# Kernel tuning notes

Measured on AMD Instinct MI355X. Metric: run time of the kernel, lower is better.

## Reference

```python
import jax, jax.numpy as jnp
import numpy as np

EPS = 1e-5

def _relu6(x):
    return jnp.clip(x, 0.0, 6.0)

def _bn(x, g, b, m, v):
    # inference-mode batchnorm folded into scale/shift
    inv = g / jnp.sqrt(v + EPS)
    return x * inv[None, :, None, None] + (b - m * inv)[None, :, None, None]

def _patch_pw(x, W):
    # per-patch 1x1 conv. x: [B,Ci,H,Wd], W: [B,Fh,Fw,Co,Ci]
    B, C, H, Wd = x.shape
    Fh, Fw = W.shape[1:3]
    ph, pw = H // Fh, Wd // Fw
    xb = x.reshape(B, C, Fh, ph, Fw, pw)
    yb = jnp.einsum('bfgoc,bcfpgq->bofpgq', W, xb)
    return yb.reshape(B, W.shape[3], H, Wd)

def _patch_dw3(x, K):
    # per-patch depthwise 3x3, reflect pad applied to the full map (halo from neighbors).
    # x: [B,C,H,Wd], K: [B,Fh,Fw,C,3,3]
    B, C, H, Wd = x.shape
    Fh, Fw = K.shape[1:3]
    ph, pw = H // Fh, Wd // Fw
    xp = jnp.pad(x, ((0, 0), (0, 0), (1, 1), (1, 1)), mode='reflect')
    acc = jnp.zeros((B, C, Fh, ph, Fw, pw), x.dtype)
    for dy in range(3):
        for dx in range(3):
            xs = xp[:, :, dy:dy + H, dx:dx + Wd].reshape(B, C, Fh, ph, Fw, pw)
            k = K[:, :, :, :, dy, dx].transpose(0, 3, 1, 2)  # [B,C,Fh,Fw]
            acc = acc + xs * k[:, :, :, None, :, None]
    return acc.reshape(B, C, H, Wd)

def setup_inputs() -> dict:
    key = jax.random.key(0)
    ks = jax.random.split(key, 16)
    B, Cin, H, Wd = 4, 64, 128, 128
    hidden, Cout, Fh, Fw = 384, 64, 16, 16
    n_params = hidden * Cin + hidden * 9 + Cout * hidden  # 52608
    return {
        'x': jax.random.normal(ks[0], (B, Cin, H, Wd), jnp.float32),
        'w': jax.random.normal(ks[1], (B, n_params, Fh, Fw), jnp.float32) * 0.05,
        'g1': jax.random.uniform(ks[2], (hidden,), jnp.float32),
        'b1': jax.random.normal(ks[3], (hidden,), jnp.float32),
        'm1': jax.random.normal(ks[4], (hidden,), jnp.float32),
        'v1': jax.random.uniform(ks[5], (hidden,), jnp.float32),
        'g2': jax.random.uniform(ks[6], (hidden,), jnp.float32),
        'b2': jax.random.normal(ks[7], (hidden,), jnp.float32),
        'm2': jax.random.normal(ks[8], (hidden,), jnp.float32),
        'v2': jax.random.uniform(ks[9], (hidden,), jnp.float32),
        'g3': jax.random.uniform(ks[10], (Cout,), jnp.float32),
        'b3': jax.random.normal(ks[11], (Cout,), jnp.float32),
        'm3': jax.random.normal(ks[12], (Cout,), jnp.float32),
        'v3': jax.random.uniform(ks[13], (Cout,), jnp.float32),
    }

def reference(x, w, g1, b1, m1, v1, g2, b2, m2, v2, g3, b3, m3, v3):
    B, Cin = x.shape[:2]
    Fh, Fw = w.shape[2:]
    hidden = g1.shape[0]
    Cout = g3.shape[0]
    n1 = hidden * Cin
    n2 = hidden * 9
    wg = w.transpose(0, 2, 3, 1)  # [B,Fh,Fw,P]
    W1 = wg[..., :n1].reshape(B, Fh, Fw, hidden, Cin)
    K2 = wg[..., n1:n1 + n2].reshape(B, Fh, Fw, hidden, 3, 3)
    W3 = wg[..., n1 + n2:].reshape(B, Fh, Fw, Cout, hidden)
    h = _relu6(_bn(_patch_pw(x, W1), g1, b1, m1, v1))
    h = _relu6(_bn(_patch_dw3(h, K2), g2, b2, m2, v2))
    h = _bn(_patch_pw(h, W3), g3, b3, m3, v3)
    return x + h  # use_res_connect: stride==1 and in_nc==out_nc
```

## Files before the change

kernel.cpp:

```cpp
#include <hip/hip_runtime.h>

#define EPSV 1e-5f

constexpr int CIN = 64, NH = 128, NW = 128, HID = 384, COUT = 64;
constexpr int N1 = HID * CIN;
constexpr int N2 = HID * 9;
constexpr int NP = N1 + N2 + COUT * HID;

using bf16x8 = __attribute__((ext_vector_type(8))) short;
using f32x4  = __attribute__((ext_vector_type(4))) float;

__device__ __forceinline__ unsigned short f2bf(float f) {
  unsigned int u = __float_as_uint(f);
  u = (u + 0x7fffu + ((u >> 16) & 1u)) >> 16;
  return (unsigned short)u;
}
__device__ __forceinline__ unsigned int pack2(float a, float b) {
  return (unsigned int)f2bf(a) | ((unsigned int)f2bf(b) << 16);
}
__device__ __forceinline__ float ulo(unsigned int u) { return __uint_as_float(u << 16); }
__device__ __forceinline__ float uhi(unsigned int u) { return __uint_as_float(u & 0xffff0000u); }
__device__ __forceinline__ float clamp6(float v) { return fminf(fmaxf(v, 0.f), 6.f); }

#define BAR_LDS()                                             \
  do {                                                        \
    asm volatile("s_waitcnt lgkmcnt(0)" ::: "memory");        \
    __builtin_amdgcn_s_barrier();                             \
  } while (0)

__global__ __launch_bounds__(256) void k0_transpose(
    const float* __restrict__ x, unsigned short* __restrict__ xT) {
  __shared__ unsigned short xls[64][66];
  const int t = threadIdx.x;
  const int xh = blockIdx.x, y = blockIdx.y, b = blockIdx.z;
#pragma unroll
  for (int it = 0; it < 4; ++it) {
    int i = it * 256 + t;
    int xq = i & 15, c = i >> 4;
    float4 v = *reinterpret_cast<const float4*>(
        &x[((size_t)(b * CIN + c) * NH + y) * NW + xh * 64 + xq * 4]);
    *(unsigned int*)&xls[c][xq * 4]     = pack2(v.x, v.y);
    *(unsigned int*)&xls[c][xq * 4 + 2] = pack2(v.z, v.w);
  }
  __syncthreads();
#pragma unroll
  for (int it = 0; it < 4; ++it) {
    int i = it * 256 + t;
    int cq = i & 15, px = i >> 4;
    ushort4 o;
    o.x = xls[cq * 4 + 0][px];
    o.y = xls[cq * 4 + 1][px];
    o.z = xls[cq * 4 + 2][px];
    o.w = xls[cq * 4 + 3][px];
    *reinterpret_cast<ushort4*>(
        &xT[((size_t)(b * NH + y) * NW + xh * 64 + px) * 64 + cq * 4]) = o;
  }
}

__global__ __launch_bounds__(256) void k1_pw1(
    const float* __restrict__ w, const unsigned short* __restrict__ xT,
    const float* __restrict__ g1, const float* __restrict__ b1,
    const float* __restrict__ m1, const float* __restrict__ v1,
    unsigned short* __restrict__ h1T) {
  __shared__ unsigned short Wpk[2048 * 8];

  const unsigned int id = blockIdx.x;
  const int fbq = id & 7;
  const unsigned int rest = id >> 3;
  const int hgrp = rest % 24, q = rest / 24;
  const int fb = q * 8 + fbq;
  const int f = fb & 15, b = fb >> 4;
  const int h0 = hgrp * 16;

  const int t = threadIdx.x;
  const int lane = t & 63, wv = t >> 6;
  const int quad = lane >> 4, nn = lane & 15;
  const int pxi = wv * 16 + nn;

#pragma unroll
  for (int it = 0; it < 8; ++it) {
    int i = it * 256 + t;
    int gq = i & 3, cp = (i >> 2) & 31, hid = i >> 7;
    const float* wp =
        &w[((size_t)b * NP + (h0 + hid) * CIN + cp * 2) * 256 + f * 16 + gq * 4];
    float4 A  = *reinterpret_cast<const float4*>(wp);
    float4 Bv = *reinterpret_cast<const float4*>(wp + 256);
    int kc = cp >> 4, qd = (cp >> 2) & 3, j = (cp & 3) * 2;
    int hs = hid ^ (2 * qd) ^ gq;
    const float* Af = (const float*)&A;
    const float* Bf = (const float*)&Bv;
#pragma unroll
    for (int k = 0; k < 4; ++k) {
      int g = gq * 4 + k;
      *(unsigned int*)&Wpk[(((g * 2 + kc) * 4 + qd) * 16 + hs) * 8 + j] =
          pack2(Af[k], Bf[k]);
    }
  }

  float iv1[4], sh1[4];
#pragma unroll
  for (int jj = 0; jj < 4; ++jj) {
    int hid = h0 + quad * 4 + jj;
    float iv = g1[hid] * rsqrtf(v1[hid] + EPSV);
    iv1[jj] = iv;
    sh1[jj] = b1[hid] - m1[hid] * iv;
  }
  __syncthreads();

  const int y = f * 8 + (pxi >> 3);
  const size_t rowbase = ((size_t)b * NH + y) * NW;

  for (int g = 0; g < 16; ++g) {
    const int xc = g * 8 + (pxi & 7);
    const unsigned short* xp = &xT[(rowbase + xc) * 64];
    f32x4 acc = {0.f, 0.f, 0.f, 0.f};
    const int hs = nn ^ (2 * quad) ^ (g >> 2);
#pragma unroll
    for (int kc = 0; kc < 2; ++kc) {
      bf16x8 af = *reinterpret_cast<const bf16x8*>(
          &Wpk[(((g * 2 + kc) * 4 + quad) * 16 + hs) * 8]);
      bf16x8 bfr = *reinterpret_cast<const bf16x8*>(&xp[kc * 32 + quad * 8]);
      acc = __builtin_amdgcn_mfma_f32_16x16x32_bf16(af, bfr, acc, 0, 0, 0);
    }
    ushort4 o;
    o.x = f2bf(clamp6(acc[0] * iv1[0] + sh1[0]));
    o.y = f2bf(clamp6(acc[1] * iv1[1] + sh1[1]));
    o.z = f2bf(clamp6(acc[2] * iv1[2] + sh1[2]));
    o.w = f2bf(clamp6(acc[3] * iv1[3] + sh1[3]));
    *reinterpret_cast<ushort4*>(&h1T[(rowbase + xc) * HID + h0 + quad * 4]) = o;
  }
}

__global__ __launch_bounds__(256, 2) void k2_fused(
    const float* __restrict__ x, const float* __restrict__ w,
    const float* __restrict__ g2, const float* __restrict__ b2v,
    const float* __restrict__ m2, const float* __restrict__ v2,
    const float* __restrict__ g3, const float* __restrict__ b3v,
    const float* __restrict__ m3, const float* __restrict__ v3,
    const unsigned short* __restrict__ h1T, float* __restrict__ out) {
  __shared__ unsigned short tile[10][34][40];
  __shared__ unsigned short h2s[256][40];
  __shared__ unsigned short W3p[512 * 8];
  __shared__ unsigned short k2w[4][9][40];
  __shared__ float iv2s[HID], sh2s[HID];

  const unsigned int id = blockIdx.x;
  const int fbq = id & 7;
  const unsigned int rest = id >> 3;
  const int gang = rest & 7, q = rest >> 3;
  const int fb = q * 8 + fbq;
  const int f = fb & 15, b = fb >> 4;
  const int gq = gang >> 1, ch = gang & 1;
  const int c0 = gq * 32;

  const int t = threadIdx.x;
  const int lane = t & 63, wv = t >> 6;
  const int quad = lane >> 4, nn = lane & 15;

  for (int i = t; i < HID; i += 256) {
    float iv = g2[i] * rsqrtf(v2[i] + EPSV);
    iv2s[i] = iv;
    sh2s[i] = b2v[i] - m2[i] * iv;
  }

  float iv3[2][4], sh3[2][4];
#pragma unroll
  for (int cot = 0; cot < 2; ++cot)
#pragma unroll
    for (int jj = 0; jj < 4; ++jj) {
      int co = ch * 32 + cot * 16 + quad * 4 + jj;
      float iv = g3[co] * rsqrtf(v3[co] + EPSV);
      iv3[cot][jj] = iv;
      sh3[cot][jj] = b3v[co] - m3[co] * iv;
    }

  f32x4 acc[2][4];
#pragma unroll
  for (int cot = 0; cot < 2; ++cot)
#pragma unroll
    for (int nt = 0; nt < 4; ++nt) acc[cot][nt] = (f32x4){0.f, 0.f, 0.f, 0.f};

  const int glt = t >> 6, rt = (t >> 3) & 7, ct = t & 7;

#define TGEOM(IDX, SRC, DST)                                          \
  {                                                                   \
    int qh = (IDX) & 3, pxid = (IDX) >> 2;                            \
    int r = pxid / 34, col = pxid - r * 34;                           \
    int yy = f * 8 - 1 + r;                                           \
    yy = (yy < 0) ? -yy : ((yy > 127) ? 254 - yy : yy);               \
    int xc = c0 - 1 + col;                                            \
    xc = (xc < 0) ? 1 : ((xc > 127) ? 126 : xc);                      \
    SRC = &h1T[(((size_t)b * NH + yy) * NW + xc) * HID + qh * 8];     \
    DST = &tile[r][col][qh * 8];                                      \
  }
  const unsigned short *ts0, *ts1, *ts2, *ts3, *ts4, *ts5;
  unsigned short *td0, *td1, *td2, *td3, *td4, *td5;
  const bool tac5 = (t < 80);
  TGEOM(t, ts0, td0);
  TGEOM(256 + t, ts1, td1);
  TGEOM(512 + t, ts2, td2);
  TGEOM(768 + t, ts3, td3);
  TGEOM(1024 + t, ts4, td4);
  {
    int idx5 = tac5 ? (1280 + t) : 1359;
    TGEOM(idx5, ts5, td5);
  }
#undef TGEOM

  const int hh1 = t / 9, tap1 = t - hh1 * 9;
  const float* ksrc1 = &w[((size_t)b * NP + N1 + t) * 256 + f * 16 + gq * 4];
  const bool kac2 = (t < 32);
  const int i2k = 256 + t;
  const int hh2 = i2k / 9, tap2 = i2k - hh2 * 9;
  const float* ksrc2 = &w[((size_t)b * NP + N1 + i2k) * 256 + f * 16 + gq * 4];

  const float *wsrc0, *wsrc1;
  unsigned int *wd00, *wd01, *wd02, *wd03, *wd10, *wd11, *wd12, *wd13;
#define W3GEOM(IT, SRC, D0, D1, D2, D3)                                   \
  {                                                                      \
    int i = (IT) * 256 + t;                                              \
    int hhp = i & 15, co = i >> 4;                                       \
    SRC = &w[((size_t)b * NP + N1 + N2 + (ch * 32 + co) * HID + hhp * 2) * \
                 256 + f * 16 + gq * 4];                                 \
    int qd = (hhp * 2) >> 3, j = (hhp * 2) & 7, cot = co >> 4,           \
        cb = co & 15;                                                    \
    D0 = (unsigned int*)&W3p[(((0 * 2 + cot) * 4 + qd) * 16 +            \
                              (cb ^ (2 * qd) ^ 0)) * 8 + j];             \
    D1 = (unsigned int*)&W3p[(((1 * 2 + cot) * 4 + qd) * 16 +            \
                              (cb ^ (2 * qd) ^ 1)) * 8 + j];             \
    D2 = (unsigned int*)&W3p[(((2 * 2 + cot) * 4 + qd) * 16 +            \
                              (cb ^ (2 * qd) ^ 2)) * 8 + j];             \
    D3 = (unsigned int*)&W3p[(((3 * 2 + cot) * 4 + qd) * 16 +            \
                              (cb ^ (2 * qd) ^ 3)) * 8 + j];             \
  }
  W3GEOM(0, wsrc0, wd00, wd01, wd02, wd03);
  W3GEOM(1, wsrc1, wd10, wd11, wd12, wd13);
#undef W3GEOM

  uint4 tr0, tr1, tr2, tr3, tr4, tr5;
  float4 kr1, kr2;
  float4 wA0, wB0, wA1, wB1;

#define PREFETCH()                                                  \
  do {                                                              \
    tr0 = *reinterpret_cast<const uint4*>(ts0); ts0 += 32;          \
    tr1 = *reinterpret_cast<const uint4*>(ts1); ts1 += 32;          \
    tr2 = *reinterpret_cast<const uint4*>(ts2); ts2 += 32;          \
    tr3 = *reinterpret_cast<const uint4*>(ts3); ts3 += 32;          \
    tr4 = *reinterpret_cast<const uint4*>(ts4); ts4 += 32;          \
    if (tac5) tr5 = *reinterpret_cast<const uint4*>(ts5);           \
    ts5 += 32;                                                      \
    kr1 = *reinterpret_cast<const float4*>(ksrc1); ksrc1 += 73728;  \
    if (kac2) kr2 = *reinterpret_cast<const float4*>(ksrc2);        \
    ksrc2 += 73728;                                                 \
    wA0 = *reinterpret_cast<const float4*>(wsrc0);                  \
    wB0 = *reinterpret_cast<const float4*>(wsrc0 + 256);            \
    wsrc0 += 8192;                                                  \
    wA1 = *reinterpret_cast<const float4*>(wsrc1);                  \
    wB1 = *reinterpret_cast<const float4*>(wsrc1 + 256);            \
    wsrc1 += 8192;                                                  \
  } while (0)

  tr5 = (uint4){0u, 0u, 0u, 0u};
  kr2 = (float4){0.f, 0.f, 0.f, 0.f};
  PREFETCH();

  for (int hc = 0; hc < 12; ++hc) {
    const int hb = hc * 32;
    BAR_LDS();

    *reinterpret_cast<uint4*>(td0) = tr0;
    *reinterpret_cast<uint4*>(td1) = tr1;
    *reinterpret_cast<uint4*>(td2) = tr2;
    *reinterpret_cast<uint4*>(td3) = tr3;
    *reinterpret_cast<uint4*>(td4) = tr4;
    if (tac5) *reinterpret_cast<uint4*>(td5) = tr5;
    k2w[0][tap1][hh1] = f2bf(kr1.x);
    k2w[1][tap1][hh1] = f2bf(kr1.y);
    k2w[2][tap1][hh1] = f2bf(kr1.z);
    k2w[3][tap1][hh1] = f2bf(kr1.w);
    if (kac2) {
      k2w[0][tap2][hh2] = f2bf(kr2.x);
      k2w[1][tap2][hh2] = f2bf(kr2.y);
      k2w[2][tap2][hh2] = f2bf(kr2.z);
      k2w[3][tap2][hh2] = f2bf(kr2.w);
    }
    *wd00 = pack2(wA0.x, wB0.x);
    *wd01 = pack2(wA0.y, wB0.y);
    *wd02 = pack2(wA0.z, wB0.z);
    *wd03 = pack2(wA0.w, wB0.w);
    *wd10 = pack2(wA1.x, wB1.x);
    *wd11 = pack2(wA1.y, wB1.y);
    *wd12 = pack2(wA1.z, wB1.z);
    *wd13 = pack2(wA1.w, wB1.w);

    BAR_LDS();

    if (hc < 11) PREFETCH();

#pragma unroll
    for (int hg = 0; hg < 4; ++hg) {
      float d[8] = {0.f, 0.f, 0.f, 0.f, 0.f, 0.f, 0.f, 0.f};
#pragma unroll
      for (int dy = 0; dy < 3; ++dy)
#pragma unroll
        for (int dx = 0; dx < 3; ++dx) {
          const uint4 tv = *reinterpret_cast<const uint4*>(
              &tile[rt + dy][glt * 8 + ct + dx][hg * 8]);
          const uint4 kv =
              *reinterpret_cast<const uint4*>(&k2w[glt][dy * 3 + dx][hg * 8]);
          d[0] += ulo(tv.x) * ulo(kv.x); d[1] += uhi(tv.x) * uhi(kv.x);
          d[2] += ulo(tv.y) * ulo(kv.y); d[3] += uhi(tv.y) * uhi(kv.y);
          d[4] += ulo(tv.z) * ulo(kv.z); d[5] += uhi(tv.z) * uhi(kv.z);
          d[6] += ulo(tv.w) * ulo(kv.w); d[7] += uhi(tv.w) * uhi(kv.w);
        }
      uint4 o4;
      unsigned int op[4];
#pragma unroll
      for (int j2 = 0; j2 < 4; ++j2) {
        int ha = hb + hg * 8 + j2 * 2;
        float oa = clamp6(d[j2 * 2] * iv2s[ha] + sh2s[ha]);
        float ob = clamp6(d[j2 * 2 + 1] * iv2s[ha + 1] + sh2s[ha + 1]);
        op[j2] = (unsigned int)f2bf(oa) | ((unsigned int)f2bf(ob) << 16);
      }
      o4.x = op[0]; o4.y = op[1]; o4.z = op[2]; o4.w = op[3];
      *reinterpret_cast<uint4*>(&h2s[t][hg * 8]) = o4;
    }

    BAR_LDS();

    {
      const int gl = wv;
      const int cop = nn ^ (2 * quad) ^ gl;
      bf16x8 a0 = *reinterpret_cast<const bf16x8*>(
          &W3p[(((gl * 2 + 0) * 4 + quad) * 16 + cop) * 8]);
      bf16x8 a1 = *reinterpret_cast<const bf16x8*>(
          &W3p[(((gl * 2 + 1) * 4 + quad) * 16 + cop) * 8]);
#pragma unroll
      for (int nt = 0; nt < 4; ++nt) {
        bf16x8 bfr = *reinterpret_cast<const bf16x8*>(
            &h2s[gl * 64 + nt * 16 + nn][quad * 8]);
        acc[0][nt] = __builtin_amdgcn_mfma_f32_16x16x32_bf16(a0, bfr, acc[0][nt], 0, 0, 0);
        acc[1][nt] = __builtin_amdgcn_mfma_f32_16x16x32_bf16(a1, bfr, acc[1][nt], 0, 0, 0);
      }
    }
  }

#pragma unroll
  for (int cot = 0; cot < 2; ++cot)
#pragma unroll
    for (int nt = 0; nt < 4; ++nt) {
      int pxl = nt * 16 + nn;
      int y = f * 8 + (pxl >> 3);
      int xc = c0 + wv * 8 + (pxl & 7);
#pragma unroll
      for (int jj = 0; jj < 4; ++jj) {
        int co = ch * 32 + cot * 16 + quad * 4 + jj;
        size_t adr = ((size_t)(b * COUT + co) * NH + y) * NW + xc;
        out[adr] = acc[cot][nt][jj] * iv3[cot][jj] + sh3[cot][jj] + x[adr];
      }
    }
}

extern "C" void kernel_launch(void* const* d_in, const int* in_sizes, int n_in,
                              void* d_out, int out_size, void* d_ws,
                              size_t ws_size, hipStream_t stream) {
  (void)in_sizes; (void)n_in; (void)out_size; (void)ws_size;
  const float* x  = (const float*)d_in[0];
  const float* w  = (const float*)d_in[1];
  const float* g1 = (const float*)d_in[2];
  const float* b1 = (const float*)d_in[3];
  const float* m1 = (const float*)d_in[4];
  const float* v1 = (const float*)d_in[5];
  const float* g2 = (const float*)d_in[6];
  const float* b2 = (const float*)d_in[7];
  const float* m2 = (const float*)d_in[8];
  const float* v2 = (const float*)d_in[9];
  const float* g3 = (const float*)d_in[10];
  const float* b3 = (const float*)d_in[11];
  const float* m3 = (const float*)d_in[12];
  const float* v3 = (const float*)d_in[13];
  float* out = (float*)d_out;
  unsigned short* h1T = (unsigned short*)d_ws;
  unsigned short* xT = (unsigned short*)d_out;

  k0_transpose<<<dim3(2, 128, 4), 256, 0, stream>>>(x, xT);
  k1_pw1<<<dim3(1536), 256, 0, stream>>>(w, xT, g1, b1, m1, v1, h1T);
  k2_fused<<<dim3(512), 256, 0, stream>>>(x, w, g2, b2, m2, v2, g3, b3, m3, v3,
                                          h1T, out);
}
```

Measured before the change: 440.1 us.

## Merge output-channel halves into one 512-thread block in fused dw+pw kernel

Each fused depthwise+pointwise block now covers all 64 output channels with 512 threads instead of two 256-thread blocks each covering 32 channels. Before, both blocks loaded the same h1 halo tile and depthwise weights and repeated the whole depthwise 3x3 computation. Now that work is done once and split across the two halves by hidden sub-group, which cuts redundant global loads and depthwise math. The cost is a larger block with more LDS for the doubled W3 buffer, half as many blocks (256), and possibly lower occupancy or a worse load balance across CUs.

```diff
diff --git a/kernel.cpp b/kernel.cpp
--- a/kernel.cpp
+++ b/kernel.cpp
@@ -131,7 +131,7 @@
   }
 }
 
-__global__ __launch_bounds__(256, 2) void k2_fused(
+__global__ __launch_bounds__(512, 2) void k2_fused(
     const float* __restrict__ x, const float* __restrict__ w,
     const float* __restrict__ g2, const float* __restrict__ b2v,
     const float* __restrict__ m2, const float* __restrict__ v2,
@@ -140,35 +140,37 @@
     const unsigned short* __restrict__ h1T, float* __restrict__ out) {
   __shared__ unsigned short tile[10][34][40];
   __shared__ unsigned short h2s[256][40];
-  __shared__ unsigned short W3p[512 * 8];
+  __shared__ unsigned short W3p[2 * 4096];
   __shared__ unsigned short k2w[4][9][40];
   __shared__ float iv2s[HID], sh2s[HID];
 
   const unsigned int id = blockIdx.x;
   const int fbq = id & 7;
   const unsigned int rest = id >> 3;
-  const int gang = rest & 7, q = rest >> 3;
+  const int gq = rest & 3, q = rest >> 2;
   const int fb = q * 8 + fbq;
   const int f = fb & 15, b = fb >> 4;
-  const int gq = gang >> 1, ch = gang & 1;
   const int c0 = gq * 32;
 
   const int t = threadIdx.x;
-  const int lane = t & 63, wv = t >> 6;
+  const int lane = t & 63;
   const int quad = lane >> 4, nn = lane & 15;
 
-  for (int i = t; i < HID; i += 256) {
+  for (int i = t; i < HID; i += 512) {
     float iv = g2[i] * rsqrtf(v2[i] + EPSV);
     iv2s[i] = iv;
     sh2s[i] = b2v[i] - m2[i] * iv;
   }
 
+  const int wv = t >> 6;
+  const int gl = wv & 3, coh = wv >> 2;
+
   float iv3[2][4], sh3[2][4];
 #pragma unroll
   for (int cot = 0; cot < 2; ++cot)
 #pragma unroll
     for (int jj = 0; jj < 4; ++jj) {
-      int co = ch * 32 + cot * 16 + quad * 4 + jj;
+      int co = coh * 32 + cot * 16 + quad * 4 + jj;
       float iv = g3[co] * rsqrtf(v3[co] + EPSV);
       iv3[cot][jj] = iv;
       sh3[cot][jj] = b3v[co] - m3[co] * iv;
@@ -180,7 +182,8 @@
 #pragma unroll
     for (int nt = 0; nt < 4; ++nt) acc[cot][nt] = (f32x4){0.f, 0.f, 0.f, 0.f};
 
-  const int glt = t >> 6, rt = (t >> 3) & 7, ct = t & 7;
+  const int px = t & 255, half = t >> 8;
+  const int glt = px >> 6, rt = (px >> 3) & 7, ct = px & 7;
 
 #define TGEOM(IDX, SRC, DST)                                          \
   {                                                                   \
@@ -193,76 +196,71 @@
     SRC = &h1T[(((size_t)b * NH + yy) * NW + xc) * HID + qh * 8];     \
     DST = &tile[r][col][qh * 8];                                      \
   }
-  const unsigned short *ts0, *ts1, *ts2, *ts3, *ts4, *ts5;
-  unsigned short *td0, *td1, *td2, *td3, *td4, *td5;
-  const bool tac5 = (t < 80);
+  const unsigned short *ts0, *ts1, *ts2;
+  unsigned short *td0, *td1, *td2;
+  const bool tac2 = (t < 336);
   TGEOM(t, ts0, td0);
-  TGEOM(256 + t, ts1, td1);
-  TGEOM(512 + t, ts2, td2);
-  TGEOM(768 + t, ts3, td3);
-  TGEOM(1024 + t, ts4, td4);
+  TGEOM(512 + t, ts1, td1);
   {
-    int idx5 = tac5 ? (1280 + t) : 1359;
-    TGEOM(idx5, ts5, td5);
+    int idx2 = tac2 ? (1024 + t) : 1359;
+    TGEOM(idx2, ts2, td2);
   }
 #undef TGEOM
 
-  const int hh1 = t / 9, tap1 = t - hh1 * 9;
-  const float* ksrc1 = &w[((size_t)b * NP + N1 + t) * 256 + f * 16 + gq * 4];
-  const bool kac2 = (t < 32);
-  const int i2k = 256 + t;
-  const int hh2 = i2k / 9, tap2 = i2k - hh2 * 9;
-  const float* ksrc2 = &w[((size_t)b * NP + N1 + i2k) * 256 + f * 16 + gq * 4];
+  const bool kac1 = (t < 288);
+  const int tk = kac1 ? t : 287;
+  const int hh1 = tk / 9, tap1 = tk - hh1 * 9;
+  const float* ksrc1 = &w[((size_t)b * NP + N1 + tk) * 256 + f * 16 + gq * 4];
 
   const float *wsrc0, *wsrc1;
   unsigned int *wd00, *wd01, *wd02, *wd03, *wd10, *wd11, *wd12, *wd13;
-#define W3GEOM(IT, SRC, D0, D1, D2, D3)                                   \
-  {                                                                      \
-    int i = (IT) * 256 + t;                                              \
-    int hhp = i & 15, co = i >> 4;                                       \
-    SRC = &w[((size_t)b * NP + N1 + N2 + (ch * 32 + co) * HID + hhp * 2) * \
-                 256 + f * 16 + gq * 4];                                 \
-    int qd = (hhp * 2) >> 3, j = (hhp * 2) & 7, cot = co >> 4,           \
-        cb = co & 15;                                                    \
-    D0 = (unsigned int*)&W3p[(((0 * 2 + cot) * 4 + qd) * 16 +            \
-                              (cb ^ (2 * qd) ^ 0)) * 8 + j];             \
-    D1 = (unsigned int*)&W3p[(((1 * 2 + cot) * 4 + qd) * 16 +            \
-                              (cb ^ (2 * qd) ^ 1)) * 8 + j];             \
-    D2 = (unsigned int*)&W3p[(((2 * 2 + cot) * 4 + qd) * 16 +            \
-                              (cb ^ (2 * qd) ^ 2)) * 8 + j];             \
-    D3 = (unsigned int*)&W3p[(((3 * 2 + cot) * 4 + qd) * 16 +            \
-                              (cb ^ (2 * qd) ^ 3)) * 8 + j];             \
+#define W3GEOM(IT, SRC, D0, D1, D2, D3)                                    \
+  {                                                                        \
+    int i = (IT) * 512 + t;                                                \
+    int hhp = i & 15, co = i >> 4;                           \
+    SRC = &w[((size_t)b * NP + N1 + N2 + co * HID + hhp * 2) * 256 +       \
+             f * 16 + gq * 4];                                             \
+    int qd = (hhp * 2) >> 3, j = (hhp * 2) & 7;                            \
+    int ch2 = co >> 5, cot = (co >> 4) & 1, cb = co & 15;                  \
+    D0 = (unsigned int*)&W3p[ch2 * 4096 +                                  \
+                             (((0 * 2 + cot) * 4 + qd) * 16 +              \
+                              (cb ^ (2 * qd) ^ 0)) * 8 + j];               \
+    D1 = (unsigned int*)&W3p[ch2 * 4096 +                                  \
+                             (((1 * 2 + cot) * 4 + qd) * 16 +              \
+                              (cb ^ (2 * qd) ^ 1)) * 8 + j];               \
+    D2 = (unsigned int*)&W3p[ch2 * 4096 +                                  \
+                             (((2 * 2 + cot) * 4 + qd) * 16 +              \
+                              (cb ^ (2 * qd) ^ 2)) * 8 + j];               \
+    D3 = (unsigned int*)&W3p[ch2 * 4096 +                                  \
+                             (((3 * 2 + cot) * 4 + qd) * 16 +              \
+                              (cb ^ (2 * qd) ^ 3)) * 8 + j];               \
   }
   W3GEOM(0, wsrc0, wd00, wd01, wd02, wd03);
   W3GEOM(1, wsrc1, wd10, wd11, wd12, wd13);
 #undef W3GEOM
 
-  uint4 tr0, tr1, tr2, tr3, tr4, tr5;
-  float4 kr1, kr2;
+  uint4 tr0, tr1, tr2;
+  float4 kr1;
   float4 wA0, wB0, wA1, wB1;
 
 #define PREFETCH()                                                  \
   do {                                                              \
     tr0 = *reinterpret_cast<const uint4*>(ts0); ts0 += 32;          \
     tr1 = *reinterpret_cast<const uint4*>(ts1); ts1 += 32;          \
-    tr2 = *reinterpret_cast<const uint4*>(ts2); ts2 += 32;          \
-    tr3 = *reinterpret_cast<const uint4*>(ts3); ts3 += 32;          \
-    tr4 = *reinterpret_cast<const uint4*>(ts4); ts4 += 32;          \
-    if (tac5) tr5 = *reinterpret_cast<const uint4*>(ts5);           \
-    ts5 += 32;                                                      \
-    kr1 = *reinterpret_cast<const float4*>(ksrc1); ksrc1 += 73728;  \
-    if (kac2) kr2 = *reinterpret_cast<const float4*>(ksrc2);        \
-    ksrc2 += 73728;                                                 \
+    if (tac2) tr2 = *reinterpret_cast<const uint4*>(ts2);           \
+    ts2 += 32;                                                      \
+    if (kac1) kr1 = *reinterpret_cast<const float4*>(ksrc1);        \
+    ksrc1 += 73728;                                   \
     wA0 = *reinterpret_cast<const float4*>(wsrc0);                  \
     wB0 = *reinterpret_cast<const float4*>(wsrc0 + 256);            \
-    wsrc0 += 8192;                                                  \
+    wsrc0 += 8192;                                      \
     wA1 = *reinterpret_cast<const float4*>(wsrc1);                  \
     wB1 = *reinterpret_cast<const float4*>(wsrc1 + 256);            \
     wsrc1 += 8192;                                                  \
   } while (0)
 
-  tr5 = (uint4){0u, 0u, 0u, 0u};
-  kr2 = (float4){0.f, 0.f, 0.f, 0.f};
+  tr2 = (uint4){0u, 0u, 0u, 0u};
+  kr1 = (float4){0.f, 0.f, 0.f, 0.f};
   PREFETCH();
 
   for (int hc = 0; hc < 12; ++hc) {
@@ -271,19 +269,12 @@
 
     *reinterpret_cast<uint4*>(td0) = tr0;
     *reinterpret_cast<uint4*>(td1) = tr1;
-    *reinterpret_cast<uint4*>(td2) = tr2;
-    *reinterpret_cast<uint4*>(td3) = tr3;
-    *reinterpret_cast<uint4*>(td4) = tr4;
-    if (tac5) *reinterpret_cast<uint4*>(td5) = tr5;
-    k2w[0][tap1][hh1] = f2bf(kr1.x);
-    k2w[1][tap1][hh1] = f2bf(kr1.y);
-    k2w[2][tap1][hh1] = f2bf(kr1.z);
-    k2w[3][tap1][hh1] = f2bf(kr1.w);
-    if (kac2) {
-      k2w[0][tap2][hh2] = f2bf(kr2.x);
-      k2w[1][tap2][hh2] = f2bf(kr2.y);
-      k2w[2][tap2][hh2] = f2bf(kr2.z);
-      k2w[3][tap2][hh2] = f2bf(kr2.w);
+    if (tac2) *reinterpret_cast<uint4*>(td2) = tr2;
+    if (kac1) {
+      k2w[0][tap1][hh1] = f2bf(kr1.x);
+      k2w[1][tap1][hh1] = f2bf(kr1.y);
+      k2w[2][tap1][hh1] = f2bf(kr1.z);
+      k2w[3][tap1][hh1] = f2bf(kr1.w);
     }
     *wd00 = pack2(wA0.x, wB0.x);
     *wd01 = pack2(wA0.y, wB0.y);
@@ -299,7 +290,8 @@
     if (hc < 11) PREFETCH();
 
 #pragma unroll
-    for (int hg = 0; hg < 4; ++hg) {
+    for (int hg2 = 0; hg2 < 2; ++hg2) {
+      const int hg = half * 2 + hg2;
       float d[8] = {0.f, 0.f, 0.f, 0.f, 0.f, 0.f, 0.f, 0.f};
 #pragma unroll
       for (int dy = 0; dy < 3; ++dy)
@@ -324,18 +316,17 @@
         op[j2] = (unsigned int)f2bf(oa) | ((unsigned int)f2bf(ob) << 16);
       }
       o4.x = op[0]; o4.y = op[1]; o4.z = op[2]; o4.w = op[3];
-      *reinterpret_cast<uint4*>(&h2s[t][hg * 8]) = o4;
+      *reinterpret_cast<uint4*>(&h2s[px][hg * 8]) = o4;
     }
 
     BAR_LDS();
 
     {
-      const int gl = wv;
       const int cop = nn ^ (2 * quad) ^ gl;
       bf16x8 a0 = *reinterpret_cast<const bf16x8*>(
-          &W3p[(((gl * 2 + 0) * 4 + quad) * 16 + cop) * 8]);
+          &W3p[coh * 4096 + (((gl * 2 + 0) * 4 + quad) * 16 + cop) * 8]);
       bf16x8 a1 = *reinterpret_cast<const bf16x8*>(
-          &W3p[(((gl * 2 + 1) * 4 + quad) * 16 + cop) * 8]);
+          &W3p[coh * 4096 + (((gl * 2 + 1) * 4 + quad) * 16 + cop) * 8]);
 #pragma unroll
       for (int nt = 0; nt < 4; ++nt) {
         bf16x8 bfr = *reinterpret_cast<const bf16x8*>(
@@ -352,10 +343,10 @@
     for (int nt = 0; nt < 4; ++nt) {
       int pxl = nt * 16 + nn;
       int y = f * 8 + (pxl >> 3);
-      int xc = c0 + wv * 8 + (pxl & 7);
+      int xc = c0 + gl * 8 + (pxl & 7);
 #pragma unroll
       for (int jj = 0; jj < 4; ++jj) {
-        int co = ch * 32 + cot * 16 + quad * 4 + jj;
+        int co = coh * 32 + cot * 16 + quad * 4 + jj;
         size_t adr = ((size_t)(b * COUT + co) * NH + y) * NW + xc;
         out[adr] = acc[cot][nt][jj] * iv3[cot][jj] + sh3[cot][jj] + x[adr];
       }
@@ -386,6 +377,6 @@
 
   k0_transpose<<<dim3(2, 128, 4), 256, 0, stream>>>(x, xT);
   k1_pw1<<<dim3(1536), 256, 0, stream>>>(w, xT, g1, b1, m1, v1, h1T);
-  k2_fused<<<dim3(512), 256, 0, stream>>>(x, w, g2, b2, m2, v2, g3, b3, m3, v3,
+  k2_fused<<<dim3(256), 512, 0, stream>>>(x, w, g2, b2, m2, v2, g3, b3, m3, v3,
                                           h1T, out);
 }
```

Measured after the change: 439.8 us. Within noise of the previous version (-0.1%).
